# Kernel optimization log

Hardware: AMD Instinct MI355X
Metric: run time of the kernel (lower is better)

The kernel has to match this reference:

```python
import jax, jax.numpy as jnp
import numpy as np

N_HIDDEN = 15


def lstm_cell(x, h, c, W_ih, W_hh, b_ih, b_hh):
    # x: [B, in], h/c: [B, H]. PyTorch LSTMCell gate order: i, f, g, o
    gates = x @ W_ih.T + h @ W_hh.T + b_ih + b_hh  # [B, 4H]
    i, f, g, o = jnp.split(gates, 4, axis=-1)
    i = jax.nn.sigmoid(i)
    f = jax.nn.sigmoid(f)
    g = jnp.tanh(g)
    o = jax.nn.sigmoid(o)
    c_new = f * c + i * g
    h_new = o * jnp.tanh(c_new)
    return h_new, c_new


def setup_inputs() -> dict:
    key = jax.random.key(0)
    ks = jax.random.split(key, 12)
    B, T, H = 4096, 1024, N_HIDDEN
    s = 1.0 / np.sqrt(H)  # torch default init bound
    u = lambda k, shape: jax.random.uniform(k, shape, jnp.float32, -s, s)
    return {
        "input": jax.random.normal(ks[0], (B, T), jnp.float32),
        "W_ih1": u(ks[1], (4 * H, 1)),
        "W_hh1": u(ks[2], (4 * H, H)),
        "b_ih1": u(ks[3], (4 * H,)),
        "b_hh1": u(ks[4], (4 * H,)),
        "W_ih2": u(ks[5], (4 * H, H)),
        "W_hh2": u(ks[6], (4 * H, H)),
        "b_ih2": u(ks[7], (4 * H,)),
        "b_hh2": u(ks[8], (4 * H,)),
        "W_lin": u(ks[9], (1, H)),
        "b_lin": u(ks[10], (1,)),
        "future": 64,
    }


def reference(input, W_ih1, W_hh1, b_ih1, b_hh1, W_ih2, W_hh2, b_ih2, b_hh2, W_lin, b_lin, future):
    B = input.shape[0]
    H = N_HIDDEN
    zeros = jnp.zeros((B, H), input.dtype)

    def step(carry, x_t):
        h1, c1, h2, c2 = carry
        h1, c1 = lstm_cell(x_t, h1, c1, W_ih1, W_hh1, b_ih1, b_hh1)
        h2, c2 = lstm_cell(h1, h2, c2, W_ih2, W_hh2, b_ih2, b_hh2)
        out = h2 @ W_lin.T + b_lin  # [B, 1]
        return (h1, c1, h2, c2), out

    xs = input.T[:, :, None]  # [T, B, 1]
    carry, outs = jax.lax.scan(step, (zeros, zeros, zeros, zeros), xs)

    last_out = outs[-1]  # [B, 1]

    def fut_step(carry, _):
        h1, c1, h2, c2, out = carry
        (h1, c1, h2, c2), out = step((h1, c1, h2, c2), out)
        return (h1, c1, h2, c2, out), out

    _, fut_outs = jax.lax.scan(fut_step, (*carry, last_out), None, length=future)

    all_outs = jnp.concatenate([outs, fut_outs], axis=0)  # [T+future, B, 1]
    return all_outs[:, :, 0].T  # [B, T+future]
```

## Files before the change

kernel.cpp:

```cpp
#include <hip/hip_runtime.h>

#define HID   15
#define TMAIN 1024
#define FUT   64
#define OUTW  (TMAIN + FUT)

typedef _Float16 v2h   __attribute__((ext_vector_type(2)));
typedef _Float16 v8h   __attribute__((ext_vector_type(8)));
typedef float    f32x4 __attribute__((ext_vector_type(4)));
typedef int      i32x4 __attribute__((ext_vector_type(4)));

__device__ __forceinline__ float rcp_(float x)  { return __builtin_amdgcn_rcpf(x); }
__device__ __forceinline__ float exp2_(float x) { return __builtin_amdgcn_exp2f(x); }

template<int I> struct ic { static constexpr int v = I; };
template<int J, int N, class F>
__device__ __forceinline__ void unroll_for(F&& f) {
    if constexpr (J < N) { f(ic<J>{}); unroll_for<J + 1, N>(f); }
}

template<int PAT>
__device__ __forceinline__ int swzi(int x) { return __builtin_amdgcn_ds_swizzle(x, PAT); }
template<int PAT>
__device__ __forceinline__ float swzf(float x) { return __int_as_float(swzi<PAT>(__float_as_int(x))); }

__device__ __forceinline__ int bpermi(int addr, int x) { return __builtin_amdgcn_ds_bpermute(addr, x); }
__device__ __forceinline__ float bpermf(int addr, float x) { return __int_as_float(bpermi(addr, __float_as_int(x))); }

template<int CTRL>
__device__ __forceinline__ int dppi(int x) {
    return __builtin_amdgcn_update_dpp(0, x, CTRL, 0xF, 0xF, true);
}

__device__ __forceinline__ v2h pkrtz(float lo, float hi) {
    return __builtin_bit_cast(v2h, __builtin_amdgcn_cvt_pkrtz(lo, hi));
}
__device__ __forceinline__ f32x4 mfma16(v8h a, v8h b, f32x4 c) {
    return __builtin_amdgcn_mfma_f32_16x16x32_f16(a, b, c, 0, 0, 0);
}
template<int I>
__device__ __forceinline__ float xel(const f32x4& a, const f32x4& b) {
    if constexpr (I < 4) return a[I]; else return b[I - 4];
}

__global__ __launch_bounds__(256)
__attribute__((amdgpu_waves_per_eu(1, 1)))
void lstm_seq_kernel(const float* __restrict__ input,
                     const float* __restrict__ W_ih1, const float* __restrict__ W_hh1,
                     const float* __restrict__ b_ih1, const float* __restrict__ b_hh1,
                     const float* __restrict__ W_ih2, const float* __restrict__ W_hh2,
                     const float* __restrict__ b_ih2, const float* __restrict__ b_hh2,
                     const float* __restrict__ W_lin, const float* __restrict__ b_lin,
                     float* __restrict__ out)
{
    const int tid  = threadIdx.x;
    const int wq   = tid >> 6;
    const int lane = tid & 63;
    const int u    = lane >> 4;
    const int c    = lane & 15;
    const int s    = c & 3;
    const int cg   = c >> 2;
    const int b0   = (blockIdx.x * 4 + wq) * 4;

    const float L2E = 1.442695040888963f;
    const float sA[4] = {-L2E, -L2E, -2.0f * L2E, -L2E};
    const float blin = b_lin[0];

    v8h   A1[4], A2[4];
    f32x4 C1[4], C2[4];
    #pragma unroll
    for (int m = 0; m < 4; ++m) {
        #pragma unroll
        for (int e = 0; e < 8; ++e) {
            const int k = (e < 4) ? (4 * u + e) : (16 + 4 * u + (e - 4));
            float v1 = 0.0f, v2 = 0.0f;
            if (c < HID) {
                const int wr = m * HID + c;
                if (k < HID)       { v1 = W_hh1[wr * HID + k]; v2 = W_ih2[wr * HID + k]; }
                else if (k == HID) { v1 = W_ih1[wr]; }
                else if (k >= 16 && k < 16 + HID) { v2 = W_hh2[wr * HID + (k - 16)]; }
            }
            float a2v = sA[m] * v2;
            if (c == 15 && m == 3 && k >= 16 && k < 16 + HID)
                a2v = W_lin[k - 16];
            A1[m][e] = (_Float16)(sA[m] * v1);
            A2[m][e] = (_Float16)a2v;
        }
        #pragma unroll
        for (int r = 0; r < 4; ++r) {
            const int U = 4 * u + r;
            float bv1 = 0.0f, bv2 = 0.0f;
            if (U < HID) {
                bv1 = sA[m] * (b_ih1[m * HID + U] + b_hh1[m * HID + U]);
                bv2 = sA[m] * (b_ih2[m * HID + U] + b_hh2[m * HID + U]);
            }
            if (u == 3 && m == 3 && r == 3) bv2 = blin;
            C1[m][r] = bv1; C2[m][r] = bv2;
        }
    }

    const int   Uown = 4 * u + cg;
    const float wl2  = (Uown < HID) ? W_lin[Uown] : 0.0f;

    const bool cgb0  = (cg & 1) != 0;
    const bool cgb1  = (cg & 2) != 0;
    const bool u3b   = (u == 3);
    const int  a32   = (lane ^ 32) << 2;

    int B0 = 0, B1 = 0, B2 = 0, B3 = 0;
    float c1v = 0.0f, c2v = 0.0f;
    float oA = 0.0f, oB = 0.0f;

    auto makeB = [&]() -> v8h {
        return __builtin_bit_cast(v8h, (i32x4){B0, B1, B2, B3});
    };

    auto gsel = [&](const f32x4& q0, const f32x4& q1, const f32x4& q2, const f32x4& q3,
                    float& g0, float& g1, float& g2, float& g3) {
        auto pick = [&](const f32x4& q) -> float {
            const float t0 = cgb0 ? q[1] : q[0];
            const float t1 = cgb0 ? q[3] : q[2];
            return cgb1 ? t1 : t0;
        };
        g0 = pick(q0); g1 = pick(q1); g2 = pick(q2); g3 = pick(q3);
    };

    auto acts = [&](float g0, float g1, float g2, float g3, float& cv) -> float {
        const float Ei = exp2_(g0);
        const float Ef = exp2_(g1);
        const float Eg = exp2_(g2);
        const float Eo = exp2_(g3);
        const float Di = 1.0f + Ei;
        const float Df = 1.0f + Ef;
        const float Dg = 1.0f + Eg;
        const float P  = Di * Dg;
        const float t  = __builtin_fmaf(-Eg, Df, Df);
        const float numer = __builtin_fmaf(cv, P, t);
        cv = numer * rcp_(P * Df);
        const float Y  = exp2_(cv * -2.885390081777927f);
        return (1.0f - Y) * rcp_((1.0f + Y) * (1.0f + Eo));
    };

    auto slots = [&](float h, float& s0, float& s1, float& s2, float& s3) {
        const int hb = __float_as_int(h);
        const float r4  = __int_as_float(dppi<0x114>(hb) | dppi<0x10C>(hb));
        const float r8  = __int_as_float(dppi<0x118>(hb) | dppi<0x108>(hb));
        const float r12 = __int_as_float(dppi<0x11C>(hb) | dppi<0x104>(hb));
        const float A0 = cgb0 ? r4  : h;
        const float A1 = cgb0 ? r12 : r8;
        const float A2 = cgb0 ? h   : r12;
        const float A3 = cgb0 ? r8  : r4;
        s0 = cgb1 ? A1 : A0;
        s1 = cgb1 ? A3 : A2;
        s2 = cgb1 ? A0 : A1;
        s3 = cgb1 ? A2 : A3;
    };

    auto pack01 = [&](float h1n, float xv) {
        float s0, s1, s2, s3; slots(h1n, s0, s1, s2, s3);
        B0 = __builtin_bit_cast(int, pkrtz(s0, s1));
        B1 = __builtin_bit_cast(int, pkrtz(s2, u3b ? xv : s3));
    };
    auto pack23 = [&](float h2n) {
        float s0, s1, s2, s3; slots(h2n, s0, s1, s2, s3);
        B2 = __builtin_bit_cast(int, pkrtz(s0, s1));
        B3 = __builtin_bit_cast(int, pkrtz(s2, s3));
    };

    auto stash = [&](auto SigC, float ov) {
        constexpr int SIG = decltype(SigC)::v;
        const bool own = (cg == (SIG & 3));
        if constexpr (SIG < 4) oA = own ? ov : oA;
        else                   oB = own ? ov : oB;
    };

    const size_t xadr   = (size_t)(b0 + s) * TMAIN;
    const size_t outb_o = (size_t)(b0 + s) * OUTW;

    auto storeChunk = [&](int chIdx, int baseOff) {
        if (u3b) {
            out[outb_o + baseOff + (size_t)chIdx * 8 + cg]     = oA;
            out[outb_o + baseOff + (size_t)chIdx * 8 + 4 + cg] = oB;
        }
    };

    auto outdot = [&](float h) -> float {
        float pv = wl2 * h;
        pv += swzf<0x101F>(pv);
        pv += swzf<0x201F>(pv);
        pv += swzf<0x401F>(pv);
        pv += bpermf(a32, pv);
        return pv + blin;
    };

    auto iterP = [&](auto Sc, float xv2) {
        constexpr int S = decltype(Sc)::v;
        const v8h Bv = makeB();
        f32x4 e0 = mfma16(A2[0], Bv, C2[0]);
        f32x4 e1 = mfma16(A2[1], Bv, C2[1]);
        f32x4 e2 = mfma16(A2[2], Bv, C2[2]);
        f32x4 e3 = mfma16(A2[3], Bv, C2[3]);
        f32x4 d0 = mfma16(A1[0], Bv, C1[0]);
        f32x4 d1 = mfma16(A1[1], Bv, C1[1]);
        f32x4 d2 = mfma16(A1[2], Bv, C1[2]);
        f32x4 d3 = mfma16(A1[3], Bv, C1[3]);

        stash(ic<(S + 7) & 7>{}, e3[3]);

        float Q0, Q1, Q2, Q3, P0, P1, P2, P3;
        gsel(e0, e1, e2, e3, Q0, Q1, Q2, Q3);
        gsel(d0, d1, d2, d3, P0, P1, P2, P3);

        const float h2n = acts(Q0, Q1, Q2, Q3, c2v);
        const float h1n = acts(P0, P1, P2, P3, c1v);

        pack01(h1n, xv2);
        pack23(h2n);
    };

    auto stepS = [&](auto Sc) {
        constexpr int S = decltype(Sc)::v;
        const v8h Bv = makeB();
        f32x4 d0 = mfma16(A1[0], Bv, C1[0]);
        f32x4 d1 = mfma16(A1[1], Bv, C1[1]);
        f32x4 d2 = mfma16(A1[2], Bv, C1[2]);
        f32x4 d3 = mfma16(A1[3], Bv, C1[3]);
        float P0, P1, P2, P3;
        gsel(d0, d1, d2, d3, P0, P1, P2, P3);
        const float h1n = acts(P0, P1, P2, P3, c1v);
        pack01(h1n, 0.0f);

        const v8h Bv2 = makeB();
        f32x4 e0 = mfma16(A2[0], Bv2, C2[0]);
        f32x4 e1 = mfma16(A2[1], Bv2, C2[1]);
        f32x4 e2 = mfma16(A2[2], Bv2, C2[2]);
        f32x4 e3 = mfma16(A2[3], Bv2, C2[3]);
        float Q0, Q1, Q2, Q3;
        gsel(e0, e1, e2, e3, Q0, Q1, Q2, Q3);
        const float h2n = acts(Q0, Q1, Q2, Q3, c2v);

        const float ov = outdot(h2n);
        stash(ic<S>{}, ov);
        const int xb = __builtin_bit_cast(int, pkrtz(0.0f, ov)) & 0xFFFF0000;
        B1 = u3b ? ((B1 & 0xFFFF) | xb) : B1;
        pack23(h2n);
    };

    f32x4 xcA = *(const f32x4*)&input[xadr];
    f32x4 xcB = *(const f32x4*)&input[xadr + 4];
    {
        B0 = B2 = B3 = 0;
        B1 = u3b ? __builtin_bit_cast(int, pkrtz(0.0f, xcA[0])) : 0;
        const v8h Bv = makeB();
        f32x4 d0 = mfma16(A1[0], Bv, C1[0]);
        f32x4 d1 = mfma16(A1[1], Bv, C1[1]);
        f32x4 d2 = mfma16(A1[2], Bv, C1[2]);
        f32x4 d3 = mfma16(A1[3], Bv, C1[3]);
        float P0, P1, P2, P3;
        gsel(d0, d1, d2, d3, P0, P1, P2, P3);
        const float h1n = acts(P0, P1, P2, P3, c1v);
        pack01(h1n, xcA[1]);
        B2 = B3 = 0;
    }

    #pragma unroll 1
    for (int ch = 0; ch < 127; ++ch) {
        const f32x4 xnA = *(const f32x4*)&input[xadr + (size_t)(ch + 1) * 8];
        const f32x4 xnB = *(const f32x4*)&input[xadr + (size_t)(ch + 1) * 8 + 4];
        iterP(ic<0>{}, xel<2>(xcA, xcB));
        if (ch > 0) storeChunk(ch - 1, 0);
        iterP(ic<1>{}, xel<3>(xcA, xcB));
        iterP(ic<2>{}, xel<4>(xcA, xcB));
        iterP(ic<3>{}, xel<5>(xcA, xcB));
        iterP(ic<4>{}, xel<6>(xcA, xcB));
        iterP(ic<5>{}, xel<7>(xcA, xcB));
        iterP(ic<6>{}, xnA[0]);
        iterP(ic<7>{}, xnA[1]);
        xcA = xnA; xcB = xnB;
    }

    {
        iterP(ic<0>{}, xel<2>(xcA, xcB));
        storeChunk(126, 0);
        iterP(ic<1>{}, xel<3>(xcA, xcB));
        iterP(ic<2>{}, xel<4>(xcA, xcB));
        iterP(ic<3>{}, xel<5>(xcA, xcB));
        iterP(ic<4>{}, xel<6>(xcA, xcB));
        iterP(ic<5>{}, xel<7>(xcA, xcB));
        iterP(ic<6>{}, 0.0f);

        const v8h Bv = makeB();
        f32x4 e0 = mfma16(A2[0], Bv, C2[0]);
        f32x4 e1 = mfma16(A2[1], Bv, C2[1]);
        f32x4 e2 = mfma16(A2[2], Bv, C2[2]);
        f32x4 e3 = mfma16(A2[3], Bv, C2[3]);
        stash(ic<6>{}, e3[3]);
        float Q0, Q1, Q2, Q3;
        gsel(e0, e1, e2, e3, Q0, Q1, Q2, Q3);
        const float h2n = acts(Q0, Q1, Q2, Q3, c2v);
        const float ov23 = outdot(h2n);
        stash(ic<7>{}, ov23);
        storeChunk(127, 0);
        const int xb = __builtin_bit_cast(int, pkrtz(0.0f, ov23)) & 0xFFFF0000;
        B1 = u3b ? ((B1 & 0xFFFF) | xb) : B1;
        pack23(h2n);
    }

    #pragma unroll 1
    for (int fc = 0; fc < FUT / 8; ++fc) {
        unroll_for<0, 8>([&](auto sc) { stepS(sc); });
        storeChunk(fc, TMAIN);
    }
}

extern "C" void kernel_launch(void* const* d_in, const int* in_sizes, int n_in,
                              void* d_out, int out_size, void* d_ws, size_t ws_size,
                              hipStream_t stream)
{
    const float* input = (const float*)d_in[0];
    const float* W_ih1 = (const float*)d_in[1];
    const float* W_hh1 = (const float*)d_in[2];
    const float* b_ih1 = (const float*)d_in[3];
    const float* b_hh1 = (const float*)d_in[4];
    const float* W_ih2 = (const float*)d_in[5];
    const float* W_hh2 = (const float*)d_in[6];
    const float* b_ih2 = (const float*)d_in[7];
    const float* b_hh2 = (const float*)d_in[8];
    const float* W_lin = (const float*)d_in[9];
    const float* b_lin = (const float*)d_in[10];

    lstm_seq_kernel<<<256, 256, 0, stream>>>(
        input, W_ih1, W_hh1, b_ih1, b_hh1,
        W_ih2, W_hh2, b_ih2, b_hh2, W_lin, b_lin,
        (float*)d_out);
}
```

Baseline: 452.1 us.

## Halve batch columns per wave and double grid to two waves per EU

Each wave now handles 2 batch rows instead of 4, with the 16 MFMA columns remapped so pairs of lanes share a row (j = c>>1, s = c&1). The grid doubles to 512 blocks and waves_per_eu is raised to 2, so two waves can interleave on each SIMD and hide the serial MFMA/transcendental latency of the recurrence. The DPP shuffles, output reduction (extra swizzle stage) and store pattern are adapted to the new mapping. The trade-off is half the useful MFMA columns per wave and a tighter register budget at two waves per EU.

```diff
diff --git a/kernel.cpp b/kernel.cpp
--- a/kernel.cpp
+++ b/kernel.cpp
@@ -44,7 +44,7 @@
 }
 
 __global__ __launch_bounds__(256)
-__attribute__((amdgpu_waves_per_eu(1, 1)))
+__attribute__((amdgpu_waves_per_eu(2, 2)))
 void lstm_seq_kernel(const float* __restrict__ input,
                      const float* __restrict__ W_ih1, const float* __restrict__ W_hh1,
                      const float* __restrict__ b_ih1, const float* __restrict__ b_hh1,
@@ -58,9 +58,9 @@
     const int lane = tid & 63;
     const int u    = lane >> 4;
     const int c    = lane & 15;
-    const int s    = c & 3;
-    const int cg   = c >> 2;
-    const int b0   = (blockIdx.x * 4 + wq) * 4;
+    const int s    = c & 1;
+    const int j    = c >> 1;
+    const int b0   = (blockIdx.x * 4 + wq) * 2;
 
     const float L2E = 1.442695040888963f;
     const float sA[4] = {-L2E, -L2E, -2.0f * L2E, -L2E};
@@ -99,17 +99,17 @@
         }
     }
 
-    const int   Uown = 4 * u + cg;
-    const float wl2  = (Uown < HID) ? W_lin[Uown] : 0.0f;
-
-    const bool cgb0  = (cg & 1) != 0;
-    const bool cgb1  = (cg & 2) != 0;
+    const int   Uown = 4 * u + (j & 3);
+    const float wl2  = (j < 4 && Uown < HID) ? W_lin[Uown] : 0.0f;
+
+    const bool jb0   = (j & 1) != 0;
+    const bool jb1   = (j & 2) != 0;
     const bool u3b   = (u == 3);
     const int  a32   = (lane ^ 32) << 2;
 
     int B0 = 0, B1 = 0, B2 = 0, B3 = 0;
     float c1v = 0.0f, c2v = 0.0f;
-    float oA = 0.0f, oB = 0.0f;
+    float oA = 0.0f;
 
     auto makeB = [&]() -> v8h {
         return __builtin_bit_cast(v8h, (i32x4){B0, B1, B2, B3});
@@ -118,9 +118,9 @@
     auto gsel = [&](const f32x4& q0, const f32x4& q1, const f32x4& q2, const f32x4& q3,
                     float& g0, float& g1, float& g2, float& g3) {
         auto pick = [&](const f32x4& q) -> float {
-            const float t0 = cgb0 ? q[1] : q[0];
-            const float t1 = cgb0 ? q[3] : q[2];
-            return cgb1 ? t1 : t0;
+            const float t0 = jb0 ? q[1] : q[0];
+            const float t1 = jb0 ? q[3] : q[2];
+            return jb1 ? t1 : t0;
         };
         g0 = pick(q0); g1 = pick(q1); g2 = pick(q2); g3 = pick(q3);
     };
@@ -143,17 +143,17 @@
 
     auto slots = [&](float h, float& s0, float& s1, float& s2, float& s3) {
         const int hb = __float_as_int(h);
-        const float r4  = __int_as_float(dppi<0x114>(hb) | dppi<0x10C>(hb));
-        const float r8  = __int_as_float(dppi<0x118>(hb) | dppi<0x108>(hb));
-        const float r12 = __int_as_float(dppi<0x11C>(hb) | dppi<0x104>(hb));
-        const float A0 = cgb0 ? r4  : h;
-        const float A1 = cgb0 ? r12 : r8;
-        const float A2 = cgb0 ? h   : r12;
-        const float A3 = cgb0 ? r8  : r4;
-        s0 = cgb1 ? A1 : A0;
-        s1 = cgb1 ? A3 : A2;
-        s2 = cgb1 ? A0 : A1;
-        s3 = cgb1 ? A2 : A3;
+        const float r2 = __int_as_float(dppi<0x112>(hb) | dppi<0x10E>(hb));
+        const float r4 = __int_as_float(dppi<0x114>(hb) | dppi<0x10C>(hb));
+        const float r6 = __int_as_float(dppi<0x116>(hb) | dppi<0x10A>(hb));
+        const float A0 = jb0 ? r2 : h;
+        const float A1 = jb0 ? r6 : r4;
+        const float A2 = jb0 ? h  : r6;
+        const float A3 = jb0 ? r4 : r2;
+        s0 = jb1 ? A1 : A0;
+        s1 = jb1 ? A3 : A2;
+        s2 = jb1 ? A0 : A1;
+        s3 = jb1 ? A2 : A3;
     };
 
     auto pack01 = [&](float h1n, float xv) {
@@ -169,23 +169,19 @@
 
     auto stash = [&](auto SigC, float ov) {
         constexpr int SIG = decltype(SigC)::v;
-        const bool own = (cg == (SIG & 3));
-        if constexpr (SIG < 4) oA = own ? ov : oA;
-        else                   oB = own ? ov : oB;
+        oA = (j == SIG) ? ov : oA;
     };
 
     const size_t xadr   = (size_t)(b0 + s) * TMAIN;
     const size_t outb_o = (size_t)(b0 + s) * OUTW;
 
     auto storeChunk = [&](int chIdx, int baseOff) {
-        if (u3b) {
-            out[outb_o + baseOff + (size_t)chIdx * 8 + cg]     = oA;
-            out[outb_o + baseOff + (size_t)chIdx * 8 + 4 + cg] = oB;
-        }
+        if (u3b) out[outb_o + baseOff + (size_t)chIdx * 8 + j] = oA;
     };
 
     auto outdot = [&](float h) -> float {
         float pv = wl2 * h;
+        pv += swzf<0x081F>(pv);
         pv += swzf<0x101F>(pv);
         pv += swzf<0x201F>(pv);
         pv += swzf<0x401F>(pv);
@@ -329,7 +325,7 @@
     const float* W_lin = (const float*)d_in[9];
     const float* b_lin = (const float*)d_in[10];
 
-    lstm_seq_kernel<<<256, 256, 0, stream>>>(
+    lstm_seq_kernel<<<512, 256, 0, stream>>>(
         input, W_ih1, W_hh1, b_ih1, b_hh1,
         W_ih2, W_hh2, b_ih2, b_hh2, W_lin, b_lin,
         (float*)d_out);
```

Result: slower. 605.0 us (+33.8%).

## Split h2 operand copies and reorder layer activations in skewed LSTM step

Applied to the files above, without the earlier changes.

Keeps two copies of the packed h2 operand: a staged copy for the layer-1 MFMAs and a fresh copy for the layer-2 MFMAs. Layer-1 activations and packing now run before layer-2, which shortens the dependency chain feeding the next step's B0/B1 operands. Packing h2 is rewritten to use one DPP plus two ds_swizzle permutes instead of the four-slot selection network. This adds registers and a different lane permutation whose correctness depends on the MFMA operand layout.

```diff
diff --git a/kernel.cpp b/kernel.cpp
--- a/kernel.cpp
+++ b/kernel.cpp
@@ -107,13 +107,11 @@
     const bool u3b   = (u == 3);
     const int  a32   = (lane ^ 32) << 2;
 
-    int B0 = 0, B1 = 0, B2 = 0, B3 = 0;
+    int B0 = 0, B1 = 0;
+    int B2s = 0, B3s = 0;
+    int B2f = 0, B3f = 0;
     float c1v = 0.0f, c2v = 0.0f;
     float oA = 0.0f, oB = 0.0f;
-
-    auto makeB = [&]() -> v8h {
-        return __builtin_bit_cast(v8h, (i32x4){B0, B1, B2, B3});
-    };
 
     auto gsel = [&](const f32x4& q0, const f32x4& q1, const f32x4& q2, const f32x4& q3,
                     float& g0, float& g1, float& g2, float& g3) {
@@ -162,9 +160,11 @@
         B1 = __builtin_bit_cast(int, pkrtz(s2, u3b ? xv : s3));
     };
     auto pack23 = [&](float h2n) {
-        float s0, s1, s2, s3; slots(h2n, s0, s1, s2, s3);
-        B2 = __builtin_bit_cast(int, pkrtz(s0, s1));
-        B3 = __builtin_bit_cast(int, pkrtz(s2, s3));
+        const int hb = __float_as_int(h2n);
+        const float hr = __int_as_float(dppi<0x104>(hb));
+        const int p = __builtin_bit_cast(int, pkrtz(h2n, hr));
+        B2f = swzi<0x0013>(p);
+        B3f = swzi<0x0113>(p);
     };
 
     auto stash = [&](auto SigC, float ov) {
@@ -195,46 +195,48 @@
 
     auto iterP = [&](auto Sc, float xv2) {
         constexpr int S = decltype(Sc)::v;
-        const v8h Bv = makeB();
-        f32x4 e0 = mfma16(A2[0], Bv, C2[0]);
-        f32x4 e1 = mfma16(A2[1], Bv, C2[1]);
-        f32x4 e2 = mfma16(A2[2], Bv, C2[2]);
-        f32x4 e3 = mfma16(A2[3], Bv, C2[3]);
-        f32x4 d0 = mfma16(A1[0], Bv, C1[0]);
-        f32x4 d1 = mfma16(A1[1], Bv, C1[1]);
-        f32x4 d2 = mfma16(A1[2], Bv, C1[2]);
-        f32x4 d3 = mfma16(A1[3], Bv, C1[3]);
+        const v8h Bd = __builtin_bit_cast(v8h, (i32x4){B0, B1, B2s, B3s});
+        f32x4 d0 = mfma16(A1[0], Bd, C1[0]);
+        f32x4 d1 = mfma16(A1[1], Bd, C1[1]);
+        f32x4 d2 = mfma16(A1[2], Bd, C1[2]);
+        f32x4 d3 = mfma16(A1[3], Bd, C1[3]);
+        const v8h Be = __builtin_bit_cast(v8h, (i32x4){B0, B1, B2f, B3f});
+        f32x4 e0 = mfma16(A2[0], Be, C2[0]);
+        f32x4 e1 = mfma16(A2[1], Be, C2[1]);
+        f32x4 e2 = mfma16(A2[2], Be, C2[2]);
+        f32x4 e3 = mfma16(A2[3], Be, C2[3]);
+
+        float P0, P1, P2, P3;
+        gsel(d0, d1, d2, d3, P0, P1, P2, P3);
+        const float h1n = acts(P0, P1, P2, P3, c1v);
+        pack01(h1n, xv2);
 
         stash(ic<(S + 7) & 7>{}, e3[3]);
-
-        float Q0, Q1, Q2, Q3, P0, P1, P2, P3;
+        float Q0, Q1, Q2, Q3;
         gsel(e0, e1, e2, e3, Q0, Q1, Q2, Q3);
-        gsel(d0, d1, d2, d3, P0, P1, P2, P3);
-
         const float h2n = acts(Q0, Q1, Q2, Q3, c2v);
-        const float h1n = acts(P0, P1, P2, P3, c1v);
-
-        pack01(h1n, xv2);
+
+        B2s = B2f; B3s = B3f;
         pack23(h2n);
     };
 
     auto stepS = [&](auto Sc) {
         constexpr int S = decltype(Sc)::v;
-        const v8h Bv = makeB();
-        f32x4 d0 = mfma16(A1[0], Bv, C1[0]);
-        f32x4 d1 = mfma16(A1[1], Bv, C1[1]);
-        f32x4 d2 = mfma16(A1[2], Bv, C1[2]);
-        f32x4 d3 = mfma16(A1[3], Bv, C1[3]);
+        const v8h Bd = __builtin_bit_cast(v8h, (i32x4){B0, B1, B2s, B3s});
+        f32x4 d0 = mfma16(A1[0], Bd, C1[0]);
+        f32x4 d1 = mfma16(A1[1], Bd, C1[1]);
+        f32x4 d2 = mfma16(A1[2], Bd, C1[2]);
+        f32x4 d3 = mfma16(A1[3], Bd, C1[3]);
         float P0, P1, P2, P3;
         gsel(d0, d1, d2, d3, P0, P1, P2, P3);
         const float h1n = acts(P0, P1, P2, P3, c1v);
         pack01(h1n, 0.0f);
 
-        const v8h Bv2 = makeB();
-        f32x4 e0 = mfma16(A2[0], Bv2, C2[0]);
-        f32x4 e1 = mfma16(A2[1], Bv2, C2[1]);
-        f32x4 e2 = mfma16(A2[2], Bv2, C2[2]);
-        f32x4 e3 = mfma16(A2[3], Bv2, C2[3]);
+        const v8h Be = __builtin_bit_cast(v8h, (i32x4){B0, B1, B2f, B3f});
+        f32x4 e0 = mfma16(A2[0], Be, C2[0]);
+        f32x4 e1 = mfma16(A2[1], Be, C2[1]);
+        f32x4 e2 = mfma16(A2[2], Be, C2[2]);
+        f32x4 e3 = mfma16(A2[3], Be, C2[3]);
         float Q0, Q1, Q2, Q3;
         gsel(e0, e1, e2, e3, Q0, Q1, Q2, Q3);
         const float h2n = acts(Q0, Q1, Q2, Q3, c2v);
@@ -243,15 +245,16 @@
         stash(ic<S>{}, ov);
         const int xb = __builtin_bit_cast(int, pkrtz(0.0f, ov)) & 0xFFFF0000;
         B1 = u3b ? ((B1 & 0xFFFF) | xb) : B1;
+        B2s = B2f; B3s = B3f;
         pack23(h2n);
     };
 
     f32x4 xcA = *(const f32x4*)&input[xadr];
     f32x4 xcB = *(const f32x4*)&input[xadr + 4];
     {
-        B0 = B2 = B3 = 0;
+        B0 = 0;
         B1 = u3b ? __builtin_bit_cast(int, pkrtz(0.0f, xcA[0])) : 0;
-        const v8h Bv = makeB();
+        const v8h Bv = __builtin_bit_cast(v8h, (i32x4){B0, B1, 0, 0});
         f32x4 d0 = mfma16(A1[0], Bv, C1[0]);
         f32x4 d1 = mfma16(A1[1], Bv, C1[1]);
         f32x4 d2 = mfma16(A1[2], Bv, C1[2]);
@@ -260,7 +263,7 @@
         gsel(d0, d1, d2, d3, P0, P1, P2, P3);
         const float h1n = acts(P0, P1, P2, P3, c1v);
         pack01(h1n, xcA[1]);
-        B2 = B3 = 0;
+        B2s = B3s = B2f = B3f = 0;
     }
 
     #pragma unroll 1
@@ -289,11 +292,11 @@
         iterP(ic<5>{}, xel<7>(xcA, xcB));
         iterP(ic<6>{}, 0.0f);
 
-        const v8h Bv = makeB();
-        f32x4 e0 = mfma16(A2[0], Bv, C2[0]);
-        f32x4 e1 = mfma16(A2[1], Bv, C2[1]);
-        f32x4 e2 = mfma16(A2[2], Bv, C2[2]);
-        f32x4 e3 = mfma16(A2[3], Bv, C2[3]);
+        const v8h Be = __builtin_bit_cast(v8h, (i32x4){B0, B1, B2f, B3f});
+        f32x4 e0 = mfma16(A2[0], Be, C2[0]);
+        f32x4 e1 = mfma16(A2[1], Be, C2[1]);
+        f32x4 e2 = mfma16(A2[2], Be, C2[2]);
+        f32x4 e3 = mfma16(A2[3], Be, C2[3]);
         stash(ic<6>{}, e3[3]);
         float Q0, Q1, Q2, Q3;
         gsel(e0, e1, e2, e3, Q0, Q1, Q2, Q3);
@@ -303,6 +306,7 @@
         storeChunk(127, 0);
         const int xb = __builtin_bit_cast(int, pkrtz(0.0f, ov23)) & 0xFFFF0000;
         B1 = u3b ? ((B1 & 0xFFFF) | xb) : B1;
+        B2s = B2f; B3s = B3f;
         pack23(h2n);
     }
 
```

Measured after the change: 415.5 us. -8.1%, faster.
